# Kernel tuning notes

Hardware: AMD Instinct MI355X
Metric: run time of the kernel (lower is better)

## Reference

```python
import jax, jax.numpy as jnp
import numpy as np

B, T, C = 4, 2048, 1024  # n_embd == input_size == 1024
H, D = 16, 64            # num_heads, head_size


def setup_inputs() -> dict:
    key = jax.random.key(0)
    ks = jax.random.split(key, 5)
    s_in = (1.0 / C) ** 0.5   # ~Linear default init scale
    s_pr = (1.0 / (H * D)) ** 0.5
    return {
        "x": jax.random.normal(ks[0], (B, T, C), dtype=jnp.float32),
        "wq": jax.random.normal(ks[1], (H, C, D), dtype=jnp.float32) * s_in,
        "wk": jax.random.normal(ks[2], (H, C, D), dtype=jnp.float32) * s_in,
        "wv": jax.random.normal(ks[3], (H, C, D), dtype=jnp.float32) * s_in,
        "w_proj": jax.random.normal(ks[4], (H * D, C), dtype=jnp.float32) * s_pr,
        "b_proj": jnp.zeros((C,), dtype=jnp.float32),
    }


def reference(x, wq, wk, wv, w_proj, b_proj):
    Bb, Tt, Cc = x.shape
    # Batched per-head projections: [B,T,C] x [H,C,D] -> [B,H,T,D]
    q = jnp.einsum("btc,hcd->bhtd", x, wq)
    k = jnp.einsum("btc,hcd->bhtd", x, wk)
    v = jnp.einsum("btc,hcd->bhtd", x, wv)
    # NOTE: original scales by C**-0.5 with C = full embedding dim (quirk preserved)
    scale = Cc ** (-0.5)
    scores = jnp.einsum("bhtd,bhsd->bhts", q, k) * scale  # [B,H,T,T]
    causal = jnp.tril(jnp.ones((Tt, Tt), dtype=bool))
    scores = jnp.where(causal, scores, -jnp.inf)
    wei = jax.nn.softmax(scores, axis=-1)
    out = jnp.einsum("bhts,bhsd->bhtd", wei, v)           # [B,H,T,D]
    out = out.transpose(0, 2, 1, 3).reshape(Bb, Tt, -1)    # concat heads [B,T,H*D]
    return out @ w_proj + b_proj                           # [B,T,C]
```

## Files before the change

kernel.cpp:

```cpp
#include <hip/hip_runtime.h>
#include <stdint.h>


typedef uint32_t u32;
typedef __bf16 bf16x8 __attribute__((ext_vector_type(8)));
typedef __bf16 bf16x4 __attribute__((ext_vector_type(4)));
typedef unsigned short us8 __attribute__((ext_vector_type(8)));
typedef float f32x4 __attribute__((ext_vector_type(4)));

#define EXP2F(x) __builtin_amdgcn_exp2f(x)

static __device__ __forceinline__ unsigned short f2bf(float f) {
  union { float f; u32 i; } cv; cv.f = f;
  u32 x = cv.i;
  u32 r = (x + 0x7fffu + ((x >> 16) & 1u)) >> 16;
  return (unsigned short)r;
}

static __device__ __forceinline__ void gload_lds16(const unsigned short* g, unsigned short* l) {
  __builtin_amdgcn_global_load_lds(
      (__attribute__((address_space(1))) u32*)g,
      (__attribute__((address_space(3))) u32*)l, 16, 0, 0);
}

#define G8_LGKM do { asm volatile("s_waitcnt lgkmcnt(0)" ::: "memory"); \
                     __builtin_amdgcn_sched_barrier(0); } while (0)

__global__ __launch_bounds__(256) void prep(
    const float* __restrict__ x, const float* __restrict__ wq,
    const float* __restrict__ wk, const float* __restrict__ wv,
    const float* __restrict__ wp, unsigned short* __restrict__ x_bf,
    unsigned short* __restrict__ wtq, unsigned short* __restrict__ wtp) {
  __shared__ unsigned short lds[64][66];
  const int b = blockIdx.x, tid = threadIdx.x;
  if (b < 4096) {
    size_t i = (size_t)(b * 256 + tid) * 8u;
    float4 a = *(const float4*)(x + i);
    float4 c = *(const float4*)(x + i + 4);
    us8 v;
    v[0] = f2bf(a.x); v[1] = f2bf(a.y); v[2] = f2bf(a.z); v[3] = f2bf(a.w);
    v[4] = f2bf(c.x); v[5] = f2bf(c.y); v[6] = f2bf(c.z); v[7] = f2bf(c.w);
    *(us8*)(x_bf + i) = v;
    return;
  }
  if (b < 4864) {
    int idx = b - 4096;
    int z = idx >> 8, rem = idx & 255;
    int h = rem >> 4, c0 = (rem & 15) << 6;
    const float* src = (z == 0) ? wq : (z == 1) ? wk : wv;
    unsigned short* d = wtq + ((size_t)z << 20);
    const float* s = src + (size_t)h * 65536u + (size_t)c0 * 64u;
#pragma unroll
    for (int it = 0; it < 16; ++it) {
      int i2 = it * 256 + tid;
      int r = i2 >> 6, dd = i2 & 63;
      lds[dd][r] = f2bf(s[r * 64 + dd]);
    }
    __syncthreads();
#pragma unroll
    for (int it = 0; it < 16; ++it) {
      int i2 = it * 256 + tid;
      int dd = i2 >> 6, r = i2 & 63;
      d[(size_t)(h * 64 + dd) * 1024u + c0 + r] = lds[dd][r];
    }
    return;
  }
  {
    int idx = b - 4864;
    int c0 = (idx >> 4) << 6, r0 = (idx & 15) << 6;
#pragma unroll
    for (int it = 0; it < 16; ++it) {
      int i2 = it * 256 + tid;
      int r = i2 >> 6, cc = i2 & 63;
      lds[cc][r] = f2bf(wp[(size_t)(r0 + r) * 1024u + c0 + cc]);
    }
    __syncthreads();
#pragma unroll
    for (int it = 0; it < 16; ++it) {
      int i2 = it * 256 + tid;
      int cc = i2 >> 6, r = i2 & 63;
      wtp[(size_t)(c0 + cc) * 1024u + r0 + r] = lds[cc][r];
    }
  }
}

static __device__ __forceinline__ void gn_stage(const unsigned short* g,
                                                unsigned short* d, int tid) {
#pragma unroll
  for (int l = 0; l < 2; ++l) {
    int cid = l * 512 + tid;
    int r = cid >> 3, c = cid & 7;
    gload_lds16(g + (size_t)r * 1024 + ((c ^ (r & 7)) << 3), d + cid * 8);
  }
}
static __device__ __forceinline__ void gn_ldA(bf16x8 af[4][2], const unsigned short* As,
                                              int wr, int l15, int lhi) {
#pragma unroll
  for (int mi = 0; mi < 4; ++mi)
#pragma unroll
    for (int ks = 0; ks < 2; ++ks) {
      int row = wr * 64 + mi * 16 + l15;
      af[mi][ks] = *(const bf16x8*)(As + row * 64 + ((((ks << 2) | lhi) ^ (row & 7)) << 3));
    }
}
static __device__ __forceinline__ void gn_ldB(bf16x8 bf[2][2], const unsigned short* Bs,
                                              int wc, int np, int l15, int lhi) {
#pragma unroll
  for (int ni = 0; ni < 2; ++ni)
#pragma unroll
    for (int ks = 0; ks < 2; ++ks) {
      int row = wc * 64 + np * 32 + ni * 16 + l15;
      bf[ni][ks] = *(const bf16x8*)(Bs + row * 64 + ((((ks << 2) | lhi) ^ (row & 7)) << 3));
    }
}
static __device__ __forceinline__ void gn_quad(f32x4 acc[4][4], bf16x8 af[4][2],
                                               bf16x8 bf[2][2], int np) {
#pragma unroll
  for (int ks = 0; ks < 2; ++ks)
#pragma unroll
    for (int mi = 0; mi < 4; ++mi)
#pragma unroll
      for (int ni = 0; ni < 2; ++ni)
        acc[mi][np * 2 + ni] = __builtin_amdgcn_mfma_f32_16x16x32_bf16(
            af[mi][ks], bf[ni][ks], acc[mi][np * 2 + ni], 0, 0, 0);
}

template <int F32OUT>
__global__ __launch_bounds__(512, 2) void gemmN(
    const unsigned short* __restrict__ A, const unsigned short* __restrict__ Bt,
    const float* __restrict__ bias, void* __restrict__ Cv,
    unsigned short* __restrict__ vt) {
  extern __shared__ __align__(16) unsigned short ldsm[];
  unsigned short* Ab = ldsm;
  unsigned short* Bb = ldsm + 16384;
  const int tid = threadIdx.x, wid = tid >> 6, lane = tid & 63;
  const int l15 = lane & 15, lhi = lane >> 4;
  const int wr = wid >> 2, wc = wid & 3;
  const int bid = blockIdx.x;
  const int mt = ((bid & 7) << 3) | ((bid >> 3) & 7);
  const int nt = bid >> 6;
  const int m0 = mt * 128, n0 = nt * 256;
  const unsigned short* Ag = A + (size_t)m0 * 1024;
  const unsigned short* Bg = Bt + (size_t)n0 * 1024;

  f32x4 acc[4][4] = {};
  bf16x8 af[4][2], b0[2][2], b1[2][2];

  gn_stage(Bg, Bb, tid);
  gn_stage(Bg + 128 * 1024, Bb + 8192, tid);
  gn_stage(Ag, Ab, tid);
  gn_stage(Ag + 64, Ab + 8192, tid);
  asm volatile("s_waitcnt vmcnt(2)" ::: "memory");
  __builtin_amdgcn_s_barrier();

  for (int j = 0; j < 8; ++j) {
    const bool last = (j == 7);
    const int kc = j * 128;
    gn_ldA(af, Ab, wr, l15, lhi);
    gn_ldB(b0, Bb, wc, 0, l15, lhi);
    gn_stage(Bg + (kc + 64), Bb + 16384, tid);
    gn_stage(Bg + 128 * 1024 + (kc + 64), Bb + 24576, tid);
    __builtin_amdgcn_s_barrier(); G8_LGKM;
    __builtin_amdgcn_s_setprio(1); gn_quad(acc, af, b0, 0); __builtin_amdgcn_s_setprio(0);
    __builtin_amdgcn_s_barrier();
    gn_ldB(b1, Bb, wc, 1, l15, lhi);
    if (!last) gn_stage(Ag + (kc + 128), Ab, tid);
    __builtin_amdgcn_s_barrier(); G8_LGKM;
    __builtin_amdgcn_s_setprio(1); gn_quad(acc, af, b1, 1); __builtin_amdgcn_s_setprio(0);
    if (last) { asm volatile("s_waitcnt vmcnt(0)" ::: "memory"); }
    else      { asm volatile("s_waitcnt vmcnt(2)" ::: "memory"); }
    __builtin_amdgcn_s_barrier();
    gn_ldA(af, Ab + 8192, wr, l15, lhi);
    gn_ldB(b0, Bb + 16384, wc, 0, l15, lhi);
    if (!last) {
      gn_stage(Bg + (kc + 128), Bb, tid);
      gn_stage(Bg + 128 * 1024 + (kc + 128), Bb + 8192, tid);
    }
    __builtin_amdgcn_s_barrier(); G8_LGKM;
    __builtin_amdgcn_s_setprio(1); gn_quad(acc, af, b0, 0); __builtin_amdgcn_s_setprio(0);
    __builtin_amdgcn_s_barrier();
    gn_ldB(b1, Bb + 16384, wc, 1, l15, lhi);
    if (!last) gn_stage(Ag + (kc + 192), Ab + 8192, tid);
    __builtin_amdgcn_s_barrier(); G8_LGKM;
    __builtin_amdgcn_s_setprio(1); gn_quad(acc, af, b1, 1); __builtin_amdgcn_s_setprio(0);
    if (!last) asm volatile("s_waitcnt vmcnt(2)" ::: "memory");
    __builtin_amdgcn_s_barrier();
  }

  if constexpr (!F32OUT) {
    if (nt >= 8) {
      unsigned short* tl = ldsm + wid * 4608;
#pragma unroll
      for (int mi = 0; mi < 4; ++mi)
#pragma unroll
        for (int ni = 0; ni < 4; ++ni)
#pragma unroll
          for (int r = 0; r < 4; ++r)
            tl[(ni * 16 + l15) * 72 + mi * 16 + lhi * 4 + r] = f2bf(acc[mi][ni][r]);
      asm volatile("s_waitcnt lgkmcnt(0)" ::: "memory");
      const int bb = m0 >> 11;
      const int bh = bb * 16 + (nt - 8) * 4 + wc;
      const int t0 = (m0 & 2047) + wr * 64;
      unsigned short* vrow = vt + (size_t)bh * 131072u + t0;
#pragma unroll
      for (int it = 0; it < 8; ++it) {
        int idx = it * 64 + lane;
        int dd = idx >> 3, tc = (idx & 7) << 3;
        *(us8*)(vrow + (size_t)dd * 2048u + tc) = *(const us8*)(tl + dd * 72 + tc);
      }
      return;
    }
  }

#pragma unroll
  for (int mi = 0; mi < 4; ++mi) {
#pragma unroll
    for (int ni = 0; ni < 4; ++ni) {
      const int n = n0 + wc * 64 + ni * 16 + l15;
      const int mr = m0 + wr * 64 + mi * 16 + lhi * 4;
      if constexpr (F32OUT) {
        float* O = (float*)Cv;
        const float b = bias[n];
#pragma unroll
        for (int r = 0; r < 4; ++r)
          O[(size_t)(mr + r) * 1024 + n] = acc[mi][ni][r] + b;
      } else {
        unsigned short* O = (unsigned short*)Cv + ((size_t)(n >> 10) << 23);
        const int nc = n & 1023;
#pragma unroll
        for (int r = 0; r < 4; ++r)
          O[(size_t)(mr + r) * 1024 + nc] = f2bf(acc[mi][ni][r]);
      }
    }
  }
}

#define QT 128
#define KVT 64
#define PSTR 72
#define SCLOG2E 0.04508422f

__global__ __launch_bounds__(512, 4) void attn_fwd(
    const unsigned short* __restrict__ Qg, const unsigned short* __restrict__ Kg,
    const unsigned short* __restrict__ Vtg, unsigned short* __restrict__ Og) {
  __shared__ __align__(16) unsigned short Kl[2][64 * 64];
  __shared__ __align__(16) unsigned short Vl[2][64 * 64];
  __shared__ __align__(16) unsigned short Pl[8][16 * PSTR];
  const int tid = threadIdx.x, wid = tid >> 6, lane = tid & 63;
  const int l15 = lane & 15, lhi = lane >> 4, x7 = lane & 7;
  const int bid = blockIdx.x;
  const int sub = bid & 63, pair = bid >> 6;
  const int bh = ((sub & 7) << 3) | (sub >> 3);
  const int qtA = pair, qtB = 15 - pair;
  const int n0 = 2 * (qtA + 1), n1 = 2 * (qtB + 1);
  const int ntot = n0 + n1;
  const size_t base = (size_t)(bh >> 4) * (2048u * 1024u) + (size_t)(bh & 15) * 64u;
  const size_t vtbase = (size_t)bh * 131072u;

  bf16x8 vones;
#pragma unroll
  for (int j = 0; j < 8; ++j) vones[j] = (__bf16)1.0f;

  auto s0_of = [&](int g) { return ((g < n0) ? g : g - n0) * KVT; };

  auto stage = [&](int bufi, int s0) {
    int q = tid;
    int r = q >> 3;
    int c = (q & 7) ^ (r & 7);
    gload_lds16(Kg + base + (size_t)(s0 + r) * 1024u + c * 8, &Kl[bufi][q * 8]);
    gload_lds16(Vtg + vtbase + (size_t)r * 2048u + s0 + c * 8, &Vl[bufi][q * 8]);
  };

  stage(0, 0);
  __syncthreads();

  int g = 0;
  for (int pass = 0; pass < 2; ++pass) {
    const int qt = pass ? qtB : qtA;
    const int nt = pass ? n1 : n0;
    const int qrow0 = qt * QT + wid * 16;

    bf16x8 qf[2];
#pragma unroll
    for (int kj = 0; kj < 2; ++kj)
      qf[kj] = *(const bf16x8*)(Qg + base +
          (size_t)(qrow0 + l15) * 1024u + kj * 32 + lhi * 8);

    f32x4 oacc[4] = {};
    f32x4 lacc = {};

    for (int kt = 0; kt < nt; ++kt, ++g) {
      const int cur = g & 1;
      const int s0 = kt * KVT;
      if (g + 1 < ntot) stage(cur ^ 1, s0_of(g + 1));
      if (s0 <= qrow0 + 15) {
        const bool notfull = (s0 + KVT - 1 > qrow0);
        const unsigned short* Kb = Kl[cur];
        const unsigned short* Vb = Vl[cur];

        f32x4 sacc[4] = {};
#pragma unroll
        for (int kj = 0; kj < 2; ++kj) {
          bf16x8 kf[4];
#pragma unroll
          for (int sj = 0; sj < 4; ++sj) {
            int r = sj * 16 + l15;
            kf[sj] = *(const bf16x8*)(&Kb[r * 64 + (((kj * 4 + lhi) ^ x7) * 8)]);
          }
#pragma unroll
          for (int sj = 0; sj < 4; ++sj)
            sacc[sj] = __builtin_amdgcn_mfma_f32_16x16x32_bf16(
                kf[sj], qf[kj], sacc[sj], 0, 0, 0);
        }

        if (notfull) {
          const int qa = qrow0 + l15;
#pragma unroll
          for (int sj = 0; sj < 4; ++sj)
#pragma unroll
            for (int r = 0; r < 4; ++r) {
              int sa = s0 + sj * 16 + lhi * 4 + r;
              sacc[sj][r] = (sa <= qa) ? sacc[sj][r] : -3e38f;
            }
        }

#pragma unroll
        for (int sj = 0; sj < 4; ++sj) {
          float p0 = EXP2F(sacc[sj][0] * SCLOG2E);
          float p1 = EXP2F(sacc[sj][1] * SCLOG2E);
          float p2 = EXP2F(sacc[sj][2] * SCLOG2E);
          float p3 = EXP2F(sacc[sj][3] * SCLOG2E);
          bf16x4 pk;
          pk[0] = (__bf16)p0; pk[1] = (__bf16)p1;
          pk[2] = (__bf16)p2; pk[3] = (__bf16)p3;
          *(bf16x4*)(&Pl[wid][l15 * PSTR + sj * 16 + lhi * 4]) = pk;
        }

#pragma unroll
        for (int kk = 0; kk < 2; ++kk) {
          bf16x8 pf, vf[4];
          pf = *(const bf16x8*)(&Pl[wid][l15 * PSTR + kk * 32 + lhi * 8]);
#pragma unroll
          for (int dj = 0; dj < 4; ++dj) {
            int r = dj * 16 + l15;
            vf[dj] = *(const bf16x8*)(&Vb[r * 64 + (((kk * 4 + lhi) ^ x7) * 8)]);
          }
#pragma unroll
          for (int dj = 0; dj < 4; ++dj)
            oacc[dj] = __builtin_amdgcn_mfma_f32_16x16x32_bf16(
                pf, vf[dj], oacc[dj], 0, 0, 0);
          lacc = __builtin_amdgcn_mfma_f32_16x16x32_bf16(pf, vones, lacc, 0, 0, 0);
        }
      }

      __syncthreads();
    }

    float rn[4];
#pragma unroll
    for (int r = 0; r < 4; ++r) rn[r] = 1.0f / lacc[r];
#pragma unroll
    for (int dj = 0; dj < 4; ++dj)
#pragma unroll
      for (int r = 0; r < 4; ++r) {
        int t = qrow0 + lhi * 4 + r;
        Og[base + (size_t)t * 1024u + dj * 16 + l15] = f2bf(oacc[dj][r] * rn[r]);
      }
  }
}

extern "C" void kernel_launch(void* const* d_in, const int* in_sizes, int n_in,
                              void* d_out, int out_size, void* d_ws, size_t ws_size,
                              hipStream_t stream) {
  const float* x  = (const float*)d_in[0];
  const float* wq = (const float*)d_in[1];
  const float* wk = (const float*)d_in[2];
  const float* wv = (const float*)d_in[3];
  const float* wp = (const float*)d_in[4];
  const float* bp = (const float*)d_in[5];
  float* out = (float*)d_out;

  unsigned short* ws   = (unsigned short*)d_ws;
  unsigned short* x_bf = ws;
  unsigned short* wtq  = ws + ((size_t)8 << 20);
  unsigned short* wtp  = ws + ((size_t)11 << 20);
  unsigned short* qkv  = ws + ((size_t)12 << 20);
  unsigned short* q    = qkv;
  unsigned short* kk   = qkv + ((size_t)8 << 20);
  unsigned short* att  = qkv + ((size_t)16 << 20);
  unsigned short* vt   = ws + ((size_t)36 << 20);

  (void)hipFuncSetAttribute(reinterpret_cast<const void*>(&gemmN<0>),
                            hipFuncAttributeMaxDynamicSharedMemorySize, 98304);
  (void)hipFuncSetAttribute(reinterpret_cast<const void*>(&gemmN<1>),
                            hipFuncAttributeMaxDynamicSharedMemorySize, 98304);

  prep<<<5120, 256, 0, stream>>>(x, wq, wk, wv, wp, x_bf, wtq, wtp);
  gemmN<0><<<768, 512, 98304, stream>>>(x_bf, wtq, nullptr, qkv, vt);
  attn_fwd<<<512, 512, 0, stream>>>(q, kk, vt, att);
  gemmN<1><<<256, 512, 98304, stream>>>(att, wtp, bp, out, nullptr);
}
```

Before: 150.2 us.

## Shrink GEMM tile to 128x128 with 4 waves and simpler double buffering

The projection GEMM kernel changes from a 128x256 tile with 8 waves to a 128x128 tile with 4 waves. Grid sizes double and LDS drops to 64KB, and the K loop becomes a plain ping-pong double buffer over 64-wide K chunks. The goal is more blocks for better occupancy and load balance on the output GEMM, which previously had only 256 blocks. In exchange, each block reuses its tiles less, global traffic rises, and the loop now waits for all loads to finish every iteration, which gives less overlap.

```diff
diff --git a/kernel.cpp b/kernel.cpp
--- a/kernel.cpp
+++ b/kernel.cpp
@@ -87,8 +87,8 @@
 static __device__ __forceinline__ void gn_stage(const unsigned short* g,
                                                 unsigned short* d, int tid) {
 #pragma unroll
-  for (int l = 0; l < 2; ++l) {
-    int cid = l * 512 + tid;
+  for (int l = 0; l < 4; ++l) {
+    int cid = l * 256 + tid;
     int r = cid >> 3, c = cid & 7;
     gload_lds16(g + (size_t)r * 1024 + ((c ^ (r & 7)) << 3), d + cid * 8);
   }
@@ -126,7 +126,7 @@
 }
 
 template <int F32OUT>
-__global__ __launch_bounds__(512, 2) void gemmN(
+__global__ __launch_bounds__(256, 2) void gemmN(
     const unsigned short* __restrict__ A, const unsigned short* __restrict__ Bt,
     const float* __restrict__ bias, void* __restrict__ Cv,
     unsigned short* __restrict__ vt) {
@@ -135,60 +135,45 @@
   unsigned short* Bb = ldsm + 16384;
   const int tid = threadIdx.x, wid = tid >> 6, lane = tid & 63;
   const int l15 = lane & 15, lhi = lane >> 4;
-  const int wr = wid >> 2, wc = wid & 3;
+  const int wr = wid >> 1, wc = wid & 1;
   const int bid = blockIdx.x;
   const int mt = ((bid & 7) << 3) | ((bid >> 3) & 7);
   const int nt = bid >> 6;
-  const int m0 = mt * 128, n0 = nt * 256;
+  const int m0 = mt * 128, n0 = nt * 128;
   const unsigned short* Ag = A + (size_t)m0 * 1024;
   const unsigned short* Bg = Bt + (size_t)n0 * 1024;
 
   f32x4 acc[4][4] = {};
   bf16x8 af[4][2], b0[2][2], b1[2][2];
 
+  gn_stage(Ag, Ab, tid);
   gn_stage(Bg, Bb, tid);
-  gn_stage(Bg + 128 * 1024, Bb + 8192, tid);
-  gn_stage(Ag, Ab, tid);
-  gn_stage(Ag + 64, Ab + 8192, tid);
-  asm volatile("s_waitcnt vmcnt(2)" ::: "memory");
+  asm volatile("s_waitcnt vmcnt(0)" ::: "memory");
   __builtin_amdgcn_s_barrier();
 
-  for (int j = 0; j < 8; ++j) {
-    const bool last = (j == 7);
-    const int kc = j * 128;
-    gn_ldA(af, Ab, wr, l15, lhi);
-    gn_ldB(b0, Bb, wc, 0, l15, lhi);
-    gn_stage(Bg + (kc + 64), Bb + 16384, tid);
-    gn_stage(Bg + 128 * 1024 + (kc + 64), Bb + 24576, tid);
+  for (int t = 0; t < 16; ++t) {
+    const bool last = (t == 15);
+    const int kc = t * 64;
+    unsigned short* As = Ab + (t & 1) * 8192;
+    unsigned short* Bs = Bb + (t & 1) * 8192;
+    unsigned short* An = Ab + ((t & 1) ^ 1) * 8192;
+    unsigned short* Bn = Bb + ((t & 1) ^ 1) * 8192;
+    gn_ldA(af, As, wr, l15, lhi);
+    gn_ldB(b0, Bs, wc, 0, l15, lhi);
+    if (!last) gn_stage(Ag + (kc + 64), An, tid);
     __builtin_amdgcn_s_barrier(); G8_LGKM;
     __builtin_amdgcn_s_setprio(1); gn_quad(acc, af, b0, 0); __builtin_amdgcn_s_setprio(0);
     __builtin_amdgcn_s_barrier();
-    gn_ldB(b1, Bb, wc, 1, l15, lhi);
-    if (!last) gn_stage(Ag + (kc + 128), Ab, tid);
+    gn_ldB(b1, Bs, wc, 1, l15, lhi);
+    if (!last) gn_stage(Bg + (kc + 64), Bn, tid);
     __builtin_amdgcn_s_barrier(); G8_LGKM;
     __builtin_amdgcn_s_setprio(1); gn_quad(acc, af, b1, 1); __builtin_amdgcn_s_setprio(0);
-    if (last) { asm volatile("s_waitcnt vmcnt(0)" ::: "memory"); }
-    else      { asm volatile("s_waitcnt vmcnt(2)" ::: "memory"); }
+    asm volatile("s_waitcnt vmcnt(0)" ::: "memory");
     __builtin_amdgcn_s_barrier();
-    gn_ldA(af, Ab + 8192, wr, l15, lhi);
-    gn_ldB(b0, Bb + 16384, wc, 0, l15, lhi);
-    if (!last) {
-      gn_stage(Bg + (kc + 128), Bb, tid);
-      gn_stage(Bg + 128 * 1024 + (kc + 128), Bb + 8192, tid);
-    }
-    __builtin_amdgcn_s_barrier(); G8_LGKM;
-    __builtin_amdgcn_s_setprio(1); gn_quad(acc, af, b0, 0); __builtin_amdgcn_s_setprio(0);
-    __builtin_amdgcn_s_barrier();
-    gn_ldB(b1, Bb + 16384, wc, 1, l15, lhi);
-    if (!last) gn_stage(Ag + (kc + 192), Ab + 8192, tid);
-    __builtin_amdgcn_s_barrier(); G8_LGKM;
-    __builtin_amdgcn_s_setprio(1); gn_quad(acc, af, b1, 1); __builtin_amdgcn_s_setprio(0);
-    if (!last) asm volatile("s_waitcnt vmcnt(2)" ::: "memory");
-    __builtin_amdgcn_s_barrier();
   }
 
   if constexpr (!F32OUT) {
-    if (nt >= 8) {
+    if (nt >= 16) {
       unsigned short* tl = ldsm + wid * 4608;
 #pragma unroll
       for (int mi = 0; mi < 4; ++mi)
@@ -199,7 +184,7 @@
             tl[(ni * 16 + l15) * 72 + mi * 16 + lhi * 4 + r] = f2bf(acc[mi][ni][r]);
       asm volatile("s_waitcnt lgkmcnt(0)" ::: "memory");
       const int bb = m0 >> 11;
-      const int bh = bb * 16 + (nt - 8) * 4 + wc;
+      const int bh = bb * 16 + (nt - 16) * 2 + wc;
       const int t0 = (m0 & 2047) + wr * 64;
       unsigned short* vrow = vt + (size_t)bh * 131072u + t0;
 #pragma unroll
@@ -391,12 +376,12 @@
   unsigned short* vt   = ws + ((size_t)36 << 20);
 
   (void)hipFuncSetAttribute(reinterpret_cast<const void*>(&gemmN<0>),
-                            hipFuncAttributeMaxDynamicSharedMemorySize, 98304);
+                            hipFuncAttributeMaxDynamicSharedMemorySize, 65536);
   (void)hipFuncSetAttribute(reinterpret_cast<const void*>(&gemmN<1>),
-                            hipFuncAttributeMaxDynamicSharedMemorySize, 98304);
+                            hipFuncAttributeMaxDynamicSharedMemorySize, 65536);
 
   prep<<<5120, 256, 0, stream>>>(x, wq, wk, wv, wp, x_bf, wtq, wtp);
-  gemmN<0><<<768, 512, 98304, stream>>>(x_bf, wtq, nullptr, qkv, vt);
+  gemmN<0><<<1536, 256, 65536, stream>>>(x_bf, wtq, nullptr, qkv, vt);
   attn_fwd<<<512, 512, 0, stream>>>(q, kk, vt, att);
-  gemmN<1><<<256, 512, 98304, stream>>>(att, wtp, bp, out, nullptr);
-}
+  gemmN<1><<<512, 256, 65536, stream>>>(att, wtp, bp, out, nullptr);
+}
```

After: 143.2 us (median of 2 runs). -4.7%, faster.
